# Kernel optimization log

Measured on AMD Instinct MI355X. Metric: run time of the kernel, lower is better.

## Reference

```python
import jax, jax.numpy as jnp
import numpy as np

IN_FEATURES = 4096
OUT_FEATURES = 12288
INT8_MAX = 127.0


def setup_inputs() -> dict:
    key = jax.random.key(0)
    kx, kw, ks, kb = jax.random.split(key, 4)
    x = jax.random.normal(kx, (8192, IN_FEATURES), dtype=jnp.float32)
    # pre-quantized int8 weight, stored [out_features, in_features] like the torch module
    weight = jax.random.randint(kw, (OUT_FEATURES, IN_FEATURES), -127, 128, dtype=jnp.int8)
    # per-output-channel weight scale, [out_features, 1]
    weight_scale = (jax.random.uniform(ks, (OUT_FEATURES, 1), dtype=jnp.float32) * 0.02 + 1e-4)
    bias = jax.random.normal(kb, (OUT_FEATURES,), dtype=jnp.float32) * 0.01
    return {"x": x, "weight": weight, "weight_scale": weight_scale, "bias": bias}


def _dynamic_int8_quant(x):
    # symmetric per-token quantization: scale = amax(|x|) / 127
    amax = jnp.max(jnp.abs(x), axis=-1, keepdims=True)  # [M, 1]
    scale = jnp.maximum(amax, 1e-8) / INT8_MAX
    x_q = jnp.clip(jnp.round(x / scale), -INT8_MAX, INT8_MAX).astype(jnp.int8)
    return x_q, scale


def reference(x, weight, weight_scale, bias):
    x_q, x_scale = _dynamic_int8_quant(x)                    # [M,K] int8, [M,1] f32
    # int8 GEMM with int32 accumulation: [M,K] @ [K,N]
    acc = jnp.matmul(x_q.astype(jnp.int32), weight.T.astype(jnp.int32))  # [M,N] int32
    # epilogue: dequant with per-token and per-channel scales, then bias add
    out = acc.astype(jnp.float32) * x_scale * weight_scale[:, 0][None, :] + bias[None, :]
    return out.astype(x.dtype)
```

## Files before the change

kernel.cpp:

```cpp
#include <hip/hip_runtime.h>
#include <stdint.h>

#define M_DIM 8192
#define K_DIM 4096
#define N_DIM 12288

typedef int v4i __attribute__((ext_vector_type(4)));

#define GLDS16(g, l)                                                         \
  __builtin_amdgcn_global_load_lds(                                          \
      (const __attribute__((address_space(1))) void*)(g),                    \
      (__attribute__((address_space(3))) void*)(l), 16, 0, 0)

#define BARRIER() asm volatile("s_barrier" ::: "memory")
#define VMCNT0() asm volatile("s_waitcnt vmcnt(0)" ::: "memory")

__global__ __launch_bounds__(256) void prep(const float* __restrict__ x,
                                            int8_t* __restrict__ xq,
                                            float* __restrict__ xs,
                                            const int* __restrict__ w32,
                                            int8_t* __restrict__ w8) {
  const int t = threadIdx.x;
  if ((int)blockIdx.x < M_DIM) {
    const int row = blockIdx.x;
    const float* xr = x + (size_t)row * K_DIM;

    float4 v[4];
    float amax = 0.f;
#pragma unroll
    for (int i = 0; i < 4; ++i) {
      v[i] = reinterpret_cast<const float4*>(xr)[t * 4 + i];
      amax = fmaxf(amax, fmaxf(fmaxf(fabsf(v[i].x), fabsf(v[i].y)),
                               fmaxf(fabsf(v[i].z), fabsf(v[i].w))));
    }
#pragma unroll
    for (int off = 32; off > 0; off >>= 1)
      amax = fmaxf(amax, __shfl_xor(amax, off));

    __shared__ float smax[4];
    if ((t & 63) == 0) smax[t >> 6] = amax;
    __syncthreads();
    amax = fmaxf(fmaxf(smax[0], smax[1]), fmaxf(smax[2], smax[3]));

    const float scale = fmaxf(amax, 1e-8f) / 127.f;

    union {
      int8_t b[16];
      v4i v;
    } p;
    const float* pv = reinterpret_cast<const float*>(v);
#pragma unroll
    for (int i = 0; i < 16; ++i) {
      float r = rintf(pv[i] / scale);
      r = fminf(127.f, fmaxf(-127.f, r));
      p.b[i] = (int8_t)(int)r;
    }
    reinterpret_cast<v4i*>(xq + (size_t)row * K_DIM)[t] = p.v;
    if (t == 0) xs[row] = scale;
  } else {
    const size_t i = (((size_t)blockIdx.x - M_DIM) * 256 + t) * 16;
    const int4* src = reinterpret_cast<const int4*>(w32 + i);
    union {
      int8_t b[16];
      v4i v;
    } p;
#pragma unroll
    for (int c = 0; c < 4; ++c) {
      int4 q = src[c];
      p.b[c * 4 + 0] = (int8_t)q.x;
      p.b[c * 4 + 1] = (int8_t)q.y;
      p.b[c * 4 + 2] = (int8_t)q.z;
      p.b[c * 4 + 3] = (int8_t)q.w;
    }
    *reinterpret_cast<v4i*>(w8 + i) = p.v;
  }
}

#define BM 256
#define BN 256
#define BKB 128
#define NTILES (K_DIM / BKB)

__global__ __launch_bounds__(512, 2) void gemm_i8(
    const int8_t* __restrict__ xq, const float* __restrict__ xs,
    const int8_t* __restrict__ w8, const float* __restrict__ wsc,
    const float* __restrict__ bias, float* __restrict__ out) {
  __shared__ __align__(16) int8_t lds[131072];

  const int t = threadIdx.x;
  const int lane = t & 63;
  const int w = t >> 6;
  const int wr = w >> 2;
  const int wc = w & 3;
  const int fr = lane & 15;
  const int kq = lane >> 4;
  const int l7 = lane & 7;

  const int bid = (int)blockIdx.x;
  const int xcd = bid & 7;
  const int q = bid >> 3;
  const int g = q >> 5;
  const int j = q & 31;
  const int rowBase = (xcd * 4 + (j >> 3)) * BM;
  const int colBase = (g * 8 + (j & 7)) * BN;

  const int srow = t >> 3;
  const int gslot = (t & 7) ^ (srow & 7);
  const int8_t* gA = xq + (size_t)(rowBase + srow) * K_DIM + gslot * 16;
  const int8_t* gB = w8 + (size_t)(colBase + srow) * K_DIM + gslot * 16;
  int8_t* ldsw = lds + w * 1024;

#define STAGE_A(c, r0, k0) \
  GLDS16(gA + (size_t)(r0) * K_DIM + (k0), ldsw + (c) * 32768 + (r0) * 128)
#define STAGE_B(c, r0, k0) \
  GLDS16(gB + (size_t)(r0) * K_DIM + (k0), ldsw + 65536 + (c) * 32768 + (r0) * 128)

#define STAGE8(d, k1)                                                         \
  STAGE_B(d, 0, k1); STAGE_B(d, 64, k1);                                      \
  STAGE_B(d, 128, k1); STAGE_B(d, 192, k1);                                   \
  STAGE_A(d, 0, k1); STAGE_A(d, 64, k1);                                      \
  STAGE_A(d, 128, k1); STAGE_A(d, 192, k1);

  const int s0_ = kq ^ l7;
  const int s1_ = s0_ ^ 4;
  const int rA = wr * 128 + fr;
  const int rB = wc * 64 + fr;

  const v4i* pA0 = (const v4i*)lds + ((rA << 3) + s0_);
  const v4i* pA1 = (const v4i*)lds + ((rA << 3) + s1_);
  const v4i* pB0 = (const v4i*)(lds + 65536) + ((rB << 3) + s0_);
  const v4i* pB1 = (const v4i*)(lds + 65536) + ((rB << 3) + s1_);

#define LDA(dst, c, mh, ks)                                                   \
  {                                                                           \
    const v4i* _p = (ks) ? pA1 : pA0;                                         \
    dst[0] = _p[((c) << 11) + (((mh) * 64 + 0) << 3)];                        \
    dst[1] = _p[((c) << 11) + (((mh) * 64 + 16) << 3)];                       \
    dst[2] = _p[((c) << 11) + (((mh) * 64 + 32) << 3)];                       \
    dst[3] = _p[((c) << 11) + (((mh) * 64 + 48) << 3)];                       \
  }
#define LDB(dst, c, ks)                                                       \
  {                                                                           \
    const v4i* _p = (ks) ? pB1 : pB0;                                         \
    dst[0] = _p[((c) << 11) + (0 << 3)];                                      \
    dst[1] = _p[((c) << 11) + (16 << 3)];                                     \
    dst[2] = _p[((c) << 11) + (32 << 3)];                                     \
    dst[3] = _p[((c) << 11) + (48 << 3)];                                     \
  }

#define MFMA_BLK(MH, A_, B_)                                                  \
  __builtin_amdgcn_s_setprio(1);                                              \
  _Pragma("unroll") for (int ni = 0; ni < 4; ++ni)                            \
      _Pragma("unroll") for (int mi = 0; mi < 4; ++mi)                        \
          acc[(MH) * 4 + mi][ni] = __builtin_amdgcn_mfma_i32_16x16x64_i8(     \
              A_[mi], B_[ni], acc[(MH) * 4 + mi][ni], 0, 0, 0);               \
  __builtin_amdgcn_s_setprio(0);

  v4i acc[8][4];
#pragma unroll
  for (int i = 0; i < 8; ++i)
#pragma unroll
    for (int jj = 0; jj < 4; ++jj) acc[i][jj] = (v4i){0, 0, 0, 0};

  v4i a0[4], a1[4], b0[4], b1[4];

#define TILE(c, d, k1)                                                        \
  STAGE8(d, k1);                                                              \
  LDA(a1, c, 1, 0);                                                           \
  MFMA_BLK(0, a0, b0);                                                        \
  LDA(a0, c, 0, 1);                                                           \
  LDB(b1, c, 1);                                                              \
  MFMA_BLK(1, a1, b0);                                                        \
  LDA(a1, c, 1, 1);                                                           \
  MFMA_BLK(0, a0, b1);                                                        \
  MFMA_BLK(1, a1, b1);                                                        \
  VMCNT0();                                                                   \
  BARRIER();                                                                  \
  LDA(a0, d, 0, 0);                                                           \
  LDB(b0, d, 0);

#define TILE_LAST(c)                                                          \
  LDA(a1, c, 1, 0);                                                           \
  MFMA_BLK(0, a0, b0);                                                        \
  LDA(a0, c, 0, 1);                                                           \
  LDB(b1, c, 1);                                                              \
  MFMA_BLK(1, a1, b0);                                                        \
  LDA(a1, c, 1, 1);                                                           \
  MFMA_BLK(0, a0, b1);                                                        \
  MFMA_BLK(1, a1, b1);

  STAGE8(0, 0);
  VMCNT0();
  BARRIER();
  LDA(a0, 0, 0, 0);
  LDB(b0, 0, 0);

  for (int tt = 0; tt < NTILES - 2; tt += 2) {
    TILE(0, 1, (tt + 1) * BKB);
    TILE(1, 0, (tt + 2) * BKB);
  }
  TILE(0, 1, (NTILES - 1) * BKB);
  TILE_LAST(1);

  const int orow0 = rowBase + wr * 128;
  const int ocol0 = colBase + wc * 64;
  const int rsub = kq * 4;
#pragma unroll
  for (int mi8 = 0; mi8 < 8; ++mi8) {
    const int r0 = orow0 + mi8 * 16 + rsub;
    float s4[4];
#pragma unroll
    for (int r = 0; r < 4; ++r) s4[r] = xs[r0 + r];
#pragma unroll
    for (int ni = 0; ni < 4; ++ni) {
      const int col = ocol0 + ni * 16 + fr;
      const float wf = wsc[col];
      const float bb = bias[col];
#pragma unroll
      for (int r = 0; r < 4; ++r)
        out[(size_t)(r0 + r) * N_DIM + col] =
            (float)acc[mi8][ni][r] * s4[r] * wf + bb;
    }
  }
}

extern "C" void kernel_launch(void* const* d_in, const int* in_sizes, int n_in,
                              void* d_out, int out_size, void* d_ws,
                              size_t ws_size, hipStream_t stream) {
  const float* x = (const float*)d_in[0];
  const int* w32 = (const int*)d_in[1];
  const float* wscale = (const float*)d_in[2];
  const float* bias = (const float*)d_in[3];
  float* out = (float*)d_out;

  int8_t* xq = (int8_t*)d_ws;
  float* xs = (float*)((char*)d_ws + (size_t)M_DIM * K_DIM);
  int8_t* w8 = (int8_t*)((char*)d_ws + (size_t)M_DIM * K_DIM + M_DIM * 4);

  const int packBlocks = (N_DIM * K_DIM) / (256 * 16);
  prep<<<M_DIM + packBlocks, 256, 0, stream>>>(x, xq, xs, w32, w8);
  gemm_i8<<<(M_DIM / BM) * (N_DIM / BN), 512, 0, stream>>>(xq, xs, w8, wscale,
                                                           bias, out);
}
```

Before: 465.4 us.

## Pre-pack weights into MFMA fragment order and load B directly to registers

```diff
diff --git a/kernel.cpp b/kernel.cpp
--- a/kernel.cpp
+++ b/kernel.cpp
@@ -19,7 +19,7 @@
                                             int8_t* __restrict__ xq,
                                             float* __restrict__ xs,
                                             const int* __restrict__ w32,
-                                            int8_t* __restrict__ w8) {
+                                            int8_t* __restrict__ w8p) {
   const int t = threadIdx.x;
   if ((int)blockIdx.x < M_DIM) {
     const int row = blockIdx.x;
@@ -58,21 +58,32 @@
     reinterpret_cast<v4i*>(xq + (size_t)row * K_DIM)[t] = p.v;
     if (t == 0) xs[row] = scale;
   } else {
-    const size_t i = (((size_t)blockIdx.x - M_DIM) * 256 + t) * 16;
-    const int4* src = reinterpret_cast<const int4*>(w32 + i);
-    union {
-      int8_t b[16];
-      v4i v;
-    } p;
-#pragma unroll
-    for (int c = 0; c < 4; ++c) {
-      int4 q = src[c];
-      p.b[c * 4 + 0] = (int8_t)q.x;
-      p.b[c * 4 + 1] = (int8_t)q.y;
-      p.b[c * 4 + 2] = (int8_t)q.z;
-      p.b[c * 4 + 3] = (int8_t)q.w;
-    }
-    *reinterpret_cast<v4i*>(w8 + i) = p.v;
+    const int i = ((int)blockIdx.x - M_DIM) * 256 + t;
+    const int nblk = i >> 10;
+    const int kblk = (i >> 4) & 63;
+    const int kq = (i >> 2) & 3;
+    const int frq = i & 3;
+    const int n0 = nblk * 16 + frq * 4;
+    const int k0 = kblk * 64 + kq * 16;
+    const int* src = w32 + (size_t)n0 * K_DIM + k0;
+    int8_t* dst = w8p + (size_t)i * 64;
+#pragma unroll
+    for (int r = 0; r < 4; ++r) {
+      union {
+        int8_t b[16];
+        v4i v;
+      } p;
+      const int4* s4 = (const int4*)(src + (size_t)r * K_DIM);
+#pragma unroll
+      for (int c = 0; c < 4; ++c) {
+        int4 q = s4[c];
+        p.b[c * 4 + 0] = (int8_t)q.x;
+        p.b[c * 4 + 1] = (int8_t)q.y;
+        p.b[c * 4 + 2] = (int8_t)q.z;
+        p.b[c * 4 + 3] = (int8_t)q.w;
+      }
+      *(v4i*)(dst + r * 16) = p.v;
+    }
   }
 }
 
@@ -83,9 +94,9 @@
 
 __global__ __launch_bounds__(512, 2) void gemm_i8(
     const int8_t* __restrict__ xq, const float* __restrict__ xs,
-    const int8_t* __restrict__ w8, const float* __restrict__ wsc,
+    const int8_t* __restrict__ w8p, const float* __restrict__ wsc,
     const float* __restrict__ bias, float* __restrict__ out) {
-  __shared__ __align__(16) int8_t lds[131072];
+  __shared__ __align__(16) int8_t lds[65536];
 
   const int t = threadIdx.x;
   const int lane = t & 63;
@@ -107,29 +118,20 @@
   const int srow = t >> 3;
   const int gslot = (t & 7) ^ (srow & 7);
   const int8_t* gA = xq + (size_t)(rowBase + srow) * K_DIM + gslot * 16;
-  const int8_t* gB = w8 + (size_t)(colBase + srow) * K_DIM + gslot * 16;
   int8_t* ldsw = lds + w * 1024;
 
 #define STAGE_A(c, r0, k0) \
   GLDS16(gA + (size_t)(r0) * K_DIM + (k0), ldsw + (c) * 32768 + (r0) * 128)
-#define STAGE_B(c, r0, k0) \
-  GLDS16(gB + (size_t)(r0) * K_DIM + (k0), ldsw + 65536 + (c) * 32768 + (r0) * 128)
-
-#define STAGE8(d, k1)                                                         \
-  STAGE_B(d, 0, k1); STAGE_B(d, 64, k1);                                      \
-  STAGE_B(d, 128, k1); STAGE_B(d, 192, k1);                                   \
-  STAGE_A(d, 0, k1); STAGE_A(d, 64, k1);                                      \
-  STAGE_A(d, 128, k1); STAGE_A(d, 192, k1);
+#define STAGE_A4(c, k0)                                                       \
+  STAGE_A(c, 0, k0); STAGE_A(c, 64, k0);                                      \
+  STAGE_A(c, 128, k0); STAGE_A(c, 192, k0);
 
   const int s0_ = kq ^ l7;
   const int s1_ = s0_ ^ 4;
   const int rA = wr * 128 + fr;
-  const int rB = wc * 64 + fr;
 
   const v4i* pA0 = (const v4i*)lds + ((rA << 3) + s0_);
   const v4i* pA1 = (const v4i*)lds + ((rA << 3) + s1_);
-  const v4i* pB0 = (const v4i*)(lds + 65536) + ((rB << 3) + s0_);
-  const v4i* pB1 = (const v4i*)(lds + 65536) + ((rB << 3) + s1_);
 
 #define LDA(dst, c, mh, ks)                                                   \
   {                                                                           \
@@ -139,21 +141,26 @@
     dst[2] = _p[((c) << 11) + (((mh) * 64 + 32) << 3)];                       \
     dst[3] = _p[((c) << 11) + (((mh) * 64 + 48) << 3)];                       \
   }
-#define LDB(dst, c, ks)                                                       \
-  {                                                                           \
-    const v4i* _p = (ks) ? pB1 : pB0;                                         \
-    dst[0] = _p[((c) << 11) + (0 << 3)];                                      \
-    dst[1] = _p[((c) << 11) + (16 << 3)];                                     \
-    dst[2] = _p[((c) << 11) + (32 << 3)];                                     \
-    dst[3] = _p[((c) << 11) + (48 << 3)];                                     \
-  }
-
-#define MFMA_BLK(MH, A_, B_)                                                  \
+
+  const int nblkBase = (colBase >> 4) + wc * 4;
+  const int8_t* gB = w8p + (size_t)nblkBase * 65536 + (size_t)lane * 16;
+
+#define LDB8(bn, k1)                                                          \
+  bn[0][0] = *(const v4i*)(gB + (size_t)(k1) * 16 + 0 * 65536);               \
+  bn[0][1] = *(const v4i*)(gB + (size_t)(k1) * 16 + 1 * 65536);               \
+  bn[0][2] = *(const v4i*)(gB + (size_t)(k1) * 16 + 2 * 65536);               \
+  bn[0][3] = *(const v4i*)(gB + (size_t)(k1) * 16 + 3 * 65536);               \
+  bn[1][0] = *(const v4i*)(gB + (size_t)(k1) * 16 + 1024 + 0 * 65536);        \
+  bn[1][1] = *(const v4i*)(gB + (size_t)(k1) * 16 + 1024 + 1 * 65536);        \
+  bn[1][2] = *(const v4i*)(gB + (size_t)(k1) * 16 + 1024 + 2 * 65536);        \
+  bn[1][3] = *(const v4i*)(gB + (size_t)(k1) * 16 + 1024 + 3 * 65536);
+
+#define MFMA_BLK(MH, A_, Bv)                                                  \
   __builtin_amdgcn_s_setprio(1);                                              \
   _Pragma("unroll") for (int ni = 0; ni < 4; ++ni)                            \
       _Pragma("unroll") for (int mi = 0; mi < 4; ++mi)                        \
           acc[(MH) * 4 + mi][ni] = __builtin_amdgcn_mfma_i32_16x16x64_i8(     \
-              A_[mi], B_[ni], acc[(MH) * 4 + mi][ni], 0, 0, 0);               \
+              A_[mi], Bv[ni], acc[(MH) * 4 + mi][ni], 0, 0, 0);               \
   __builtin_amdgcn_s_setprio(0);
 
   v4i acc[8][4];
@@ -162,45 +169,44 @@
 #pragma unroll
     for (int jj = 0; jj < 4; ++jj) acc[i][jj] = (v4i){0, 0, 0, 0};
 
-  v4i a0[4], a1[4], b0[4], b1[4];
-
-#define TILE(c, d, k1)                                                        \
-  STAGE8(d, k1);                                                              \
+  v4i a0[4], a1[4];
+  v4i bA[2][4], bB[2][4];
+
+#define TILE(c, d, k1, bc, bn)                                                \
+  STAGE_A4(d, k1);                                                            \
+  LDB8(bn, k1);                                                               \
   LDA(a1, c, 1, 0);                                                           \
-  MFMA_BLK(0, a0, b0);                                                        \
+  MFMA_BLK(0, a0, bc[0]);                                                     \
   LDA(a0, c, 0, 1);                                                           \
-  LDB(b1, c, 1);                                                              \
-  MFMA_BLK(1, a1, b0);                                                        \
+  MFMA_BLK(1, a1, bc[0]);                                                     \
   LDA(a1, c, 1, 1);                                                           \
-  MFMA_BLK(0, a0, b1);                                                        \
-  MFMA_BLK(1, a1, b1);                                                        \
+  MFMA_BLK(0, a0, bc[1]);                                                     \
+  MFMA_BLK(1, a1, bc[1]);                                                     \
   VMCNT0();                                                                   \
   BARRIER();                                                                  \
-  LDA(a0, d, 0, 0);                                                           \
-  LDB(b0, d, 0);
-
-#define TILE_LAST(c)                                                          \
+  LDA(a0, d, 0, 0);
+
+#define TILE_LAST(c, bc)                                                      \
   LDA(a1, c, 1, 0);                                                           \
-  MFMA_BLK(0, a0, b0);                                                        \
+  MFMA_BLK(0, a0, bc[0]);                                                     \
   LDA(a0, c, 0, 1);                                                           \
-  LDB(b1, c, 1);                                                              \
-  MFMA_BLK(1, a1, b0);                                                        \
+  MFMA_BLK(1, a1, bc[0]);                                                     \
   LDA(a1, c, 1, 1);                                                           \
-  MFMA_BLK(0, a0, b1);                                                        \
-  MFMA_BLK(1, a1, b1);
-
-  STAGE8(0, 0);
+  MFMA_BLK(0, a0, bc[1]);                                                     \
+  MFMA_BLK(1, a1, bc[1]);
+
+  STAGE_A4(0, 0);
+  LDB8(bA, 0);
   VMCNT0();
   BARRIER();
   LDA(a0, 0, 0, 0);
-  LDB(b0, 0, 0);
 
   for (int tt = 0; tt < NTILES - 2; tt += 2) {
-    TILE(0, 1, (tt + 1) * BKB);
-    TILE(1, 0, (tt + 2) * BKB);
-  }
-  TILE(0, 1, (NTILES - 1) * BKB);
-  TILE_LAST(1);
+    TILE(0, 1, (tt + 1) * BKB, bA, bB);
+    TILE(1, 0, (tt + 2) * BKB, bB, bA);
+  }
+  TILE(0, 1, (NTILES - 1) * BKB, bA, bB);
+  TILE_LAST(1, bB);
 
   const int orow0 = rowBase + wr * 128;
   const int ocol0 = colBase + wc * 64;
@@ -235,10 +241,10 @@
 
   int8_t* xq = (int8_t*)d_ws;
   float* xs = (float*)((char*)d_ws + (size_t)M_DIM * K_DIM);
-  int8_t* w8 = (int8_t*)((char*)d_ws + (size_t)M_DIM * K_DIM + M_DIM * 4);
-
-  const int packBlocks = (N_DIM * K_DIM) / (256 * 16);
-  prep<<<M_DIM + packBlocks, 256, 0, stream>>>(x, xq, xs, w32, w8);
-  gemm_i8<<<(M_DIM / BM) * (N_DIM / BN), 512, 0, stream>>>(xq, xs, w8, wscale,
+  int8_t* w8p = (int8_t*)((char*)d_ws + (size_t)M_DIM * K_DIM + M_DIM * 4);
+
+  const int packBlocks = (N_DIM * K_DIM) / (256 * 64);
+  prep<<<M_DIM + packBlocks, 256, 0, stream>>>(x, xq, xs, w32, w8p);
+  gemm_i8<<<(M_DIM / BM) * (N_DIM / BN), 512, 0, stream>>>(xq, xs, w8p, wscale,
                                                            bias, out);
 }
```

Measured after the change: 499.3 us. +7.3%, slower.
